# Optimization experiments

Measured on AMD Instinct MI355X. Metric: run time of the kernel, lower is better.

The kernel has to match this reference:

```python
import jax, jax.numpy as jnp
import numpy as np
from jax import lax

B, S, H = 2, 2048, 768
FF = 1536
E = 8
TOP_K = 2


def setup_inputs() -> dict:
    key = jax.random.key(0)
    k1, k2, k3, k4 = jax.random.split(key, 4)
    hidden_states = jax.random.normal(k1, (B, S, H), dtype=jnp.float32)
    # torch init: weight.normal_() for experts; nn.Linear default init for gate (approx normal here is fine for a numerics baseline)
    gate_w = jax.random.normal(k2, (E, H), dtype=jnp.float32) * 0.02
    w_fc = jax.random.normal(k3, (E, FF, H), dtype=jnp.float32) * 0.02
    w_proj = jax.random.normal(k4, (E, H, FF), dtype=jnp.float32) * 0.02
    return {"hidden_states": hidden_states, "gate_w": gate_w, "w_fc": w_fc, "w_proj": w_proj}


def reference(hidden_states, gate_w, w_fc, w_proj):
    b, s, h = hidden_states.shape
    x = hidden_states.reshape(-1, h)                      # [T, H]
    # --- top-k gating (logits in float32, as in the torch code) ---
    logits = (x @ gate_w.T).astype(jnp.float32)           # [T, E]
    top_logits, top_idx = lax.top_k(logits, TOP_K)        # [T, K]
    gates = jax.nn.softmax(top_logits, axis=1).astype(x.dtype)  # [T, K]
    # combined per-token/per-expert gate: g[t,e] = sum_k gates[t,k]*[idx[t,k]==e]
    onehot = jax.nn.one_hot(top_idx, E, dtype=x.dtype)    # [T, K, E]
    g = jnp.einsum('tk,tke->te', gates, onehot)           # [T, E]
    # --- experts: gather + per-expert GEMM + gated scatter-add combine ---
    # Equivalent math: tokens with zero gate for expert e contribute nothing,
    # so compute each expert on all tokens and weight by g[:, e].
    out = jnp.zeros_like(x)
    for e in range(E):  # fixed small loop over experts (structurally distinct weights)
        hmid = jax.nn.gelu(x @ w_fc[e].T, approximate=False)   # [T, FF] (torch gelu = erf form)
        out = out + g[:, e:e + 1] * (hmid @ w_proj[e].T)       # [T, H]
    out = out.reshape(b, s, h)
    return out, logits
```

## Files before the change

### kernel.cpp

```cpp
#include <hip/hip_runtime.h>
#include <hip/hip_bf16.h>
#include <math.h>
#include <stdint.h>

#define TOKENS 4096
#define HDIM   768
#define FFDIM  1536
#define NEXP   8
#define NCT    12
#define WMAX   768
#define GEMM_GRID 768

typedef __attribute__((ext_vector_type(8))) short bf16x8;
typedef __attribute__((ext_vector_type(4))) float f32x4;

__device__ __forceinline__ unsigned short f2bf(float f) {
    union { float f; uint32_t u; } c; c.f = f;
    uint32_t u = c.u;
    uint32_t r = (u + 0x7FFFu + ((u >> 16) & 1u)) >> 16;
    return (unsigned short)r;
}

__device__ __forceinline__ void gload_lds16(const void* g, void* l) {
    __builtin_amdgcn_global_load_lds(
        (const __attribute__((address_space(1))) void*)g,
        (__attribute__((address_space(3))) void*)l, 16, 0, 0);
}

__global__ void cast_bf16_2(const float* __restrict__ s1, unsigned short* __restrict__ d1,
                            const float* __restrict__ s2, unsigned short* __restrict__ d2,
                            int n4) {
    int stride = gridDim.x * blockDim.x;
    for (int i = blockIdx.x * blockDim.x + threadIdx.x; i < 2 * n4; i += stride) {
        const float4* s = (i < n4) ? (const float4*)s1 : (const float4*)s2;
        ushort4* d = (i < n4) ? (ushort4*)d1 : (ushort4*)d2;
        int j = (i < n4) ? i : i - n4;
        float4 v = s[j];
        ushort4 o;
        o.x = f2bf(v.x); o.y = f2bf(v.y); o.z = f2bf(v.z); o.w = f2bf(v.w);
        d[j] = o;
    }
}

__global__ __launch_bounds__(256) void gating(
    const float* __restrict__ x, const float* __restrict__ gw,
    float* __restrict__ logits,
    int* __restrict__ tok_e, float* __restrict__ tok_g,
    unsigned short* __restrict__ x_bf, float* __restrict__ outp)
{
    float4 zz = make_float4(0.f, 0.f, 0.f, 0.f);
#pragma unroll
    for (int j = 0; j < 3; j++)
        ((float4*)outp)[blockIdx.x * 768 + j * 256 + threadIdx.x] = zz;

    int t = blockIdx.x * 4 + (threadIdx.x >> 6);
    int lane = threadIdx.x & 63;
    const float4* xt = (const float4*)(x + (size_t)t * HDIM);
    const float4* gw4 = (const float4*)gw;
    ushort4* xbt = (ushort4*)(x_bf + (size_t)t * HDIM);
    float acc[NEXP];
#pragma unroll
    for (int e = 0; e < NEXP; e++) acc[e] = 0.f;
#pragma unroll
    for (int it = 0; it < 3; it++) {
        int i = lane + it * 64;
        float4 xv = xt[i];
        ushort4 o;
        o.x = f2bf(xv.x); o.y = f2bf(xv.y); o.z = f2bf(xv.z); o.w = f2bf(xv.w);
        xbt[i] = o;
#pragma unroll
        for (int e = 0; e < NEXP; e++) {
            float4 wv = gw4[e * 192 + i];
            acc[e] += xv.x * wv.x + xv.y * wv.y + xv.z * wv.z + xv.w * wv.w;
        }
    }
#pragma unroll
    for (int e = 0; e < NEXP; e++) {
#pragma unroll
        for (int off = 32; off > 0; off >>= 1)
            acc[e] += __shfl_xor(acc[e], off);
    }
    if (lane == 0) {
        float4 l0 = make_float4(acc[0], acc[1], acc[2], acc[3]);
        float4 l1 = make_float4(acc[4], acc[5], acc[6], acc[7]);
        float4* lp = (float4*)(logits + (size_t)t * NEXP);
        lp[0] = l0; lp[1] = l1;
        int i0 = 0; float v0 = acc[0];
#pragma unroll
        for (int e = 1; e < NEXP; e++) if (acc[e] > v0) { v0 = acc[e]; i0 = e; }
        int i1 = -1; float v1 = -3.4e38f;
#pragma unroll
        for (int e = 0; e < NEXP; e++) if (e != i0 && acc[e] > v1) { v1 = acc[e]; i1 = e; }
        float g0 = 1.f / (1.f + expf(v1 - v0));
        tok_e[t * 2] = i0; tok_e[t * 2 + 1] = i1;
        tok_g[t * 2] = g0; tok_g[t * 2 + 1] = 1.f - g0;
    }
}

__global__ __launch_bounds__(1024) void build_lists(
    const int* __restrict__ tok_e, const float* __restrict__ tok_g,
    int* __restrict__ counts, int* __restrict__ bases, int* __restrict__ fill,
    int* __restrict__ work,
    int* __restrict__ entries, float* __restrict__ gates)
{
    __shared__ unsigned long long wlo[16], whi[16];
    __shared__ int scnt[8];
    int tid = threadIdx.x;
    int lane = tid & 63, wid = tid >> 6;

    int eL[8]; float gL[8];
    int4 ea = ((const int4*)tok_e)[tid * 2];
    int4 eb = ((const int4*)tok_e)[tid * 2 + 1];
    float4 ga = ((const float4*)tok_g)[tid * 2];
    float4 gb = ((const float4*)tok_g)[tid * 2 + 1];
    eL[0] = ea.x; eL[1] = ea.y; eL[2] = ea.z; eL[3] = ea.w;
    eL[4] = eb.x; eL[5] = eb.y; eL[6] = eb.z; eL[7] = eb.w;
    gL[0] = ga.x; gL[1] = ga.y; gL[2] = ga.z; gL[3] = ga.w;
    gL[4] = gb.x; gL[5] = gb.y; gL[6] = gb.z; gL[7] = gb.w;

    unsigned long long clo = 0, chi = 0;
#pragma unroll
    for (int j = 0; j < 8; j++) {
        int e = eL[j];
        unsigned long long one = 1ull << ((e & 3) * 16);
        if (e < 4) clo += one; else chi += one;
    }
    unsigned long long ilo = clo, ihi = chi;
#pragma unroll
    for (int s = 1; s < 64; s <<= 1) {
        unsigned long long t1 = __shfl_up(ilo, s);
        unsigned long long t2 = __shfl_up(ihi, s);
        if (lane >= s) { ilo += t1; ihi += t2; }
    }
    if (lane == 63) { wlo[wid] = ilo; whi[wid] = ihi; }
    __syncthreads();
    if (tid == 0) {
        unsigned long long rl = 0, rh = 0;
#pragma unroll
        for (int i = 0; i < 16; i++) {
            unsigned long long a = wlo[i], b = whi[i];
            wlo[i] = rl; whi[i] = rh;
            rl += a; rh += b;
        }
        int c[8];
#pragma unroll
        for (int e = 0; e < 4; e++) {
            c[e]     = (int)((rl >> (e * 16)) & 0xFFFF);
            c[e + 4] = (int)((rh >> (e * 16)) & 0xFFFF);
        }
        int b = 0;
#pragma unroll
        for (int e = 0; e < NEXP; e++) {
            scnt[e] = c[e]; counts[e] = c[e]; bases[e] = b; b += c[e];
            fill[e] = ((c[e] + 127) >> 7) * NCT;
        }
    }
    __syncthreads();
    if (tid < NEXP * NCT) {
        int e = tid / NCT, ct = tid % NCT;
        int rts = (scnt[e] + 127) >> 7;
        for (int r = 0; r < rts; r++)
            work[(ct * rts + r) * 8 + e] = (ct << 20) | (e << 16) | (r << 7);
    }
    unsigned long long rlo = wlo[wid] + (ilo - clo);
    unsigned long long rhi = whi[wid] + (ihi - chi);
#pragma unroll
    for (int j = 0; j < 8; j++) {
        int e = eL[j];
        int sh = (e & 3) * 16;
        unsigned long long one = 1ull << sh;
        int slot;
        if (e < 4) { slot = (int)((rlo >> sh) & 0xFFFF); rlo += one; }
        else       { slot = (int)((rhi >> sh) & 0xFFFF); rhi += one; }
        entries[e * TOKENS + slot] = tid * 8 + j;
        gates[e * TOKENS + slot]   = gL[j];
    }
}

template<int KD, int ND, int TN, bool IS_FC>
__global__ __launch_bounds__(256) void moe_gemm(
    const unsigned short* __restrict__ Asrc,
    const unsigned short* __restrict__ Bsrc,
    const int* __restrict__ counts,
    const int* __restrict__ bases,
    const int* __restrict__ fill,
    const int* __restrict__ work,
    const int* __restrict__ entries,
    const float* __restrict__ gates,
    unsigned short* __restrict__ hmid,
    float* __restrict__ outp)
{
    constexpr int AJ = TN / 32;
    constexpr int CB = TN / 32;
    int bkt = blockIdx.x & 7;
    int nfill = fill[bkt];

    int tid = threadIdx.x;
    int w = tid >> 6;
    int l = tid & 63;
    int sg = l & 7;
    int lr8 = l >> 3;
    int lo = l & 15;
    int q  = l >> 4;
    int wr = w >> 1, wc = w & 1;

    __shared__ __align__(16) unsigned short sA[128 * 64];
    __shared__ __align__(16) unsigned short sB[TN * 64];

    int aOff[4][2], bOff[AJ][2];
#pragma unroll
    for (int i = 0; i < 4; i++) {
        int m = wr * 64 + i * 16 + lo;
#pragma unroll
        for (int s = 0; s < 2; s++)
            aOff[i][s] = m * 64 + ((s * 4 + q) ^ (m & 7)) * 8;
    }
#pragma unroll
    for (int j = 0; j < AJ; j++) {
        int n = wc * (TN / 2) + j * 16 + lo;
#pragma unroll
        for (int s = 0; s < 2; s++)
            bOff[j][s] = n * 64 + ((s * 4 + q) ^ (n & 7)) * 8;
    }

    for (int p = blockIdx.x >> 3; p < nfill; p += GEMM_GRID / 8) {
        int pk   = work[p * 8 + bkt];
        int ct   = pk >> 20;
        int e    = (pk >> 16) & 0xF;
        int row0 = pk & 0xFFFF;
        int n_e  = counts[e];
        int ebase = bases[e];
        int n0 = ct * TN;
        const int* lst = entries + e * TOKENS;

        const unsigned short* Ag[4];
        int aLds[4];
#pragma unroll
        for (int c = 0; c < 4; c++) {
            int rr = w * 32 + c * 8 + lr8;
            int gr = row0 + rr;
            int id = gr < n_e ? gr : n_e - 1;
            size_t arow = IS_FC ? (size_t)(lst[id] >> 1) : (size_t)(ebase + id);
            Ag[c] = Asrc + arow * KD + (size_t)((sg ^ (rr & 7)) * 8);
            aLds[c] = (w * 32 + c * 8) * 64;
        }
        const unsigned short* Bg[CB];
        int bLds[CB];
#pragma unroll
        for (int c = 0; c < CB; c++) {
            int rr = w * (TN / 4) + c * 8 + lr8;
            Bg[c] = Bsrc + ((size_t)e * ND + n0 + rr) * KD + (size_t)((sg ^ (rr & 7)) * 8);
            bLds[c] = (w * (TN / 4) + c * 8) * 64;
        }

        f32x4 acc[4][AJ];
#pragma unroll
        for (int i = 0; i < 4; i++)
#pragma unroll
            for (int j = 0; j < AJ; j++) acc[i][j] = (f32x4){0.f, 0.f, 0.f, 0.f};

        for (int k0 = 0; k0 < KD; k0 += 64) {
#pragma unroll
            for (int c = 0; c < 4; c++) gload_lds16(Ag[c] + k0, sA + aLds[c]);
#pragma unroll
            for (int c = 0; c < CB; c++) gload_lds16(Bg[c] + k0, sB + bLds[c]);
            __syncthreads();
#pragma unroll
            for (int s = 0; s < 2; s++) {
                bf16x8 a[4], b[AJ];
#pragma unroll
                for (int i = 0; i < 4; i++) a[i] = *(const bf16x8*)(sA + aOff[i][s]);
#pragma unroll
                for (int j = 0; j < AJ; j++) b[j] = *(const bf16x8*)(sB + bOff[j][s]);
#pragma unroll
                for (int i = 0; i < 4; i++)
#pragma unroll
                    for (int j = 0; j < AJ; j++)
                        acc[i][j] = __builtin_amdgcn_mfma_f32_16x16x32_bf16(a[i], b[j], acc[i][j], 0, 0, 0);
            }
            __syncthreads();
        }

#pragma unroll
        for (int i = 0; i < 4; i++) {
            int rowB = row0 + wr * 64 + i * 16 + q * 4;
#pragma unroll
            for (int rr = 0; rr < 4; rr++) {
                int orow = rowB + rr;
                if (orow < n_e) {
                    if (IS_FC) {
                        size_t hrow = (size_t)(ebase + orow);
#pragma unroll
                        for (int j = 0; j < AJ; j++) {
                            float v = acc[i][j][rr];
                            v = 0.5f * v * (1.f + erff(v * 0.70710678118654752f));
                            hmid[hrow * ND + n0 + wc * (TN / 2) + j * 16 + lo] = f2bf(v);
                        }
                    } else {
                        int token = lst[orow] >> 1;
                        float g = gates[e * TOKENS + orow];
#pragma unroll
                        for (int j = 0; j < AJ; j++) {
                            atomicAdd(&outp[(size_t)token * ND + n0 + wc * (TN / 2) + j * 16 + lo],
                                      acc[i][j][rr] * g);
                        }
                    }
                }
            }
        }
    }
}

extern "C" void kernel_launch(void* const* d_in, const int* in_sizes, int n_in,
                              void* d_out, int out_size, void* d_ws, size_t ws_size,
                              hipStream_t stream) {
    const float* x     = (const float*)d_in[0];
    const float* gw    = (const float*)d_in[1];
    const float* wfc   = (const float*)d_in[2];
    const float* wproj = (const float*)d_in[3];
    float* outp   = (float*)d_out;
    float* logits = outp + (size_t)TOKENS * HDIM;

    char* ws = (char*)d_ws;
    int*   counts  = (int*)ws;
    int*   bases   = (int*)(ws + 64);
    int*   fill    = (int*)(ws + 128);
    int*   work    = (int*)(ws + 256);
    size_t off = 256 + (size_t)WMAX * 8 * 4;
    int*   entries = (int*)(ws + off);
    float* gates   = (float*)(ws + off + NEXP * TOKENS * 4);
    off += 2ull * NEXP * TOKENS * 4;
    int*   tok_e   = (int*)(ws + off);   off += (size_t)TOKENS * 2 * 4;
    float* tok_g   = (float*)(ws + off); off += (size_t)TOKENS * 2 * 4;
    unsigned short* x_bf   = (unsigned short*)(ws + off); off += (size_t)TOKENS * HDIM * 2;
    unsigned short* wfc_bf = (unsigned short*)(ws + off); off += (size_t)NEXP * FFDIM * HDIM * 2;
    unsigned short* wpj_bf = (unsigned short*)(ws + off); off += (size_t)NEXP * HDIM * FFDIM * 2;
    unsigned short* hmid   = (unsigned short*)(ws + off);

    cast_bf16_2<<<2048, 256, 0, stream>>>(wfc, wfc_bf, wproj, wpj_bf,
                                          NEXP * FFDIM * HDIM / 4);
    gating<<<TOKENS / 4, 256, 0, stream>>>(x, gw, logits, tok_e, tok_g, x_bf, outp);
    build_lists<<<1, 1024, 0, stream>>>(tok_e, tok_g, counts, bases, fill, work,
                                        entries, gates);
    moe_gemm<HDIM, FFDIM, 128, true ><<<GEMM_GRID, 256, 0, stream>>>(
        x_bf, wfc_bf, counts, bases, fill, work, entries, gates, hmid, outp);
    moe_gemm<FFDIM, HDIM, 64, false><<<GEMM_GRID, 256, 0, stream>>>(
        hmid, wpj_bf, counts, bases, fill, work, entries, gates, hmid, outp);
}
```

Before: 235.0 us.

## Replace list-building kernel with atomic slot assignment in gating and derived schedule

Drops the single-block build_lists kernel. Gating now appends each token to per-expert lists with global atomics, and the counters are zeroed inside the cast kernel. The GEMM blocks derive their work tiles, expert base offsets and row ranges straight from the counts, which removes one launch and the precomputed work table. The grid grows to 1024 blocks with a launch_bounds occupancy hint. The token order inside each expert list becomes nondeterministic, so the atomicAdd accumulation order changes, and the many contended atomics on eight counters may add some serialization.

```diff
diff --git a/kernel.cpp b/kernel.cpp
--- a/kernel.cpp
+++ b/kernel.cpp
@@ -7,9 +7,8 @@
 #define HDIM   768
 #define FFDIM  1536
 #define NEXP   8
-#define NCT    12
-#define WMAX   768
-#define GEMM_GRID 768
+#define GEMM_GRID 1024
+#define SLOTS (GEMM_GRID / 8)
 
 typedef __attribute__((ext_vector_type(8))) short bf16x8;
 typedef __attribute__((ext_vector_type(4))) float f32x4;
@@ -29,7 +28,8 @@
 
 __global__ void cast_bf16_2(const float* __restrict__ s1, unsigned short* __restrict__ d1,
                             const float* __restrict__ s2, unsigned short* __restrict__ d2,
-                            int n4) {
+                            int n4, int* __restrict__ counts) {
+    if (blockIdx.x == 0 && threadIdx.x < NEXP) counts[threadIdx.x] = 0;
     int stride = gridDim.x * blockDim.x;
     for (int i = blockIdx.x * blockDim.x + threadIdx.x; i < 2 * n4; i += stride) {
         const float4* s = (i < n4) ? (const float4*)s1 : (const float4*)s2;
@@ -45,7 +45,7 @@
 __global__ __launch_bounds__(256) void gating(
     const float* __restrict__ x, const float* __restrict__ gw,
     float* __restrict__ logits,
-    int* __restrict__ tok_e, float* __restrict__ tok_g,
+    int* __restrict__ counts, int* __restrict__ entries, float* __restrict__ gates,
     unsigned short* __restrict__ x_bf, float* __restrict__ outp)
 {
     float4 zz = make_float4(0.f, 0.f, 0.f, 0.f);
@@ -92,99 +92,20 @@
 #pragma unroll
         for (int e = 0; e < NEXP; e++) if (e != i0 && acc[e] > v1) { v1 = acc[e]; i1 = e; }
         float g0 = 1.f / (1.f + expf(v1 - v0));
-        tok_e[t * 2] = i0; tok_e[t * 2 + 1] = i1;
-        tok_g[t * 2] = g0; tok_g[t * 2 + 1] = 1.f - g0;
-    }
-}
-
-__global__ __launch_bounds__(1024) void build_lists(
-    const int* __restrict__ tok_e, const float* __restrict__ tok_g,
-    int* __restrict__ counts, int* __restrict__ bases, int* __restrict__ fill,
-    int* __restrict__ work,
-    int* __restrict__ entries, float* __restrict__ gates)
-{
-    __shared__ unsigned long long wlo[16], whi[16];
-    __shared__ int scnt[8];
-    int tid = threadIdx.x;
-    int lane = tid & 63, wid = tid >> 6;
-
-    int eL[8]; float gL[8];
-    int4 ea = ((const int4*)tok_e)[tid * 2];
-    int4 eb = ((const int4*)tok_e)[tid * 2 + 1];
-    float4 ga = ((const float4*)tok_g)[tid * 2];
-    float4 gb = ((const float4*)tok_g)[tid * 2 + 1];
-    eL[0] = ea.x; eL[1] = ea.y; eL[2] = ea.z; eL[3] = ea.w;
-    eL[4] = eb.x; eL[5] = eb.y; eL[6] = eb.z; eL[7] = eb.w;
-    gL[0] = ga.x; gL[1] = ga.y; gL[2] = ga.z; gL[3] = ga.w;
-    gL[4] = gb.x; gL[5] = gb.y; gL[6] = gb.z; gL[7] = gb.w;
-
-    unsigned long long clo = 0, chi = 0;
-#pragma unroll
-    for (int j = 0; j < 8; j++) {
-        int e = eL[j];
-        unsigned long long one = 1ull << ((e & 3) * 16);
-        if (e < 4) clo += one; else chi += one;
-    }
-    unsigned long long ilo = clo, ihi = chi;
-#pragma unroll
-    for (int s = 1; s < 64; s <<= 1) {
-        unsigned long long t1 = __shfl_up(ilo, s);
-        unsigned long long t2 = __shfl_up(ihi, s);
-        if (lane >= s) { ilo += t1; ihi += t2; }
-    }
-    if (lane == 63) { wlo[wid] = ilo; whi[wid] = ihi; }
-    __syncthreads();
-    if (tid == 0) {
-        unsigned long long rl = 0, rh = 0;
-#pragma unroll
-        for (int i = 0; i < 16; i++) {
-            unsigned long long a = wlo[i], b = whi[i];
-            wlo[i] = rl; whi[i] = rh;
-            rl += a; rh += b;
-        }
-        int c[8];
-#pragma unroll
-        for (int e = 0; e < 4; e++) {
-            c[e]     = (int)((rl >> (e * 16)) & 0xFFFF);
-            c[e + 4] = (int)((rh >> (e * 16)) & 0xFFFF);
-        }
-        int b = 0;
-#pragma unroll
-        for (int e = 0; e < NEXP; e++) {
-            scnt[e] = c[e]; counts[e] = c[e]; bases[e] = b; b += c[e];
-            fill[e] = ((c[e] + 127) >> 7) * NCT;
-        }
-    }
-    __syncthreads();
-    if (tid < NEXP * NCT) {
-        int e = tid / NCT, ct = tid % NCT;
-        int rts = (scnt[e] + 127) >> 7;
-        for (int r = 0; r < rts; r++)
-            work[(ct * rts + r) * 8 + e] = (ct << 20) | (e << 16) | (r << 7);
-    }
-    unsigned long long rlo = wlo[wid] + (ilo - clo);
-    unsigned long long rhi = whi[wid] + (ihi - chi);
-#pragma unroll
-    for (int j = 0; j < 8; j++) {
-        int e = eL[j];
-        int sh = (e & 3) * 16;
-        unsigned long long one = 1ull << sh;
-        int slot;
-        if (e < 4) { slot = (int)((rlo >> sh) & 0xFFFF); rlo += one; }
-        else       { slot = (int)((rhi >> sh) & 0xFFFF); rhi += one; }
-        entries[e * TOKENS + slot] = tid * 8 + j;
-        gates[e * TOKENS + slot]   = gL[j];
-    }
-}
-
-template<int KD, int ND, int TN, bool IS_FC>
-__global__ __launch_bounds__(256) void moe_gemm(
+        int s0 = atomicAdd(&counts[i0], 1);
+        int s1 = atomicAdd(&counts[i1], 1);
+        entries[i0 * TOKENS + s0] = t * 2;
+        gates  [i0 * TOKENS + s0] = g0;
+        entries[i1 * TOKENS + s1] = t * 2 + 1;
+        gates  [i1 * TOKENS + s1] = 1.f - g0;
+    }
+}
+
+template<int KD, int ND, int TN, int NCTP, bool IS_FC>
+__global__ __launch_bounds__(256, 4) void moe_gemm(
     const unsigned short* __restrict__ Asrc,
     const unsigned short* __restrict__ Bsrc,
     const int* __restrict__ counts,
-    const int* __restrict__ bases,
-    const int* __restrict__ fill,
-    const int* __restrict__ work,
     const int* __restrict__ entries,
     const float* __restrict__ gates,
     unsigned short* __restrict__ hmid,
@@ -192,8 +113,20 @@
 {
     constexpr int AJ = TN / 32;
     constexpr int CB = TN / 32;
-    int bkt = blockIdx.x & 7;
-    int nfill = fill[bkt];
+    int bkt  = blockIdx.x & 7;
+    int slot = blockIdx.x >> 3;
+
+    int cs[NEXP];
+#pragma unroll
+    for (int e = 0; e < NEXP; e++) cs[e] = counts[e];
+    int n_e = cs[bkt];
+    int rts = (n_e + 127) >> 7;
+    int nfill = rts * NCTP;
+    if (slot >= nfill) return;
+    int ebase = 0;
+#pragma unroll
+    for (int e = 0; e < NEXP; e++) if (e < bkt) ebase += cs[e];
+    const int* lst = entries + bkt * TOKENS;
 
     int tid = threadIdx.x;
     int w = tid >> 6;
@@ -223,15 +156,11 @@
             bOff[j][s] = n * 64 + ((s * 4 + q) ^ (n & 7)) * 8;
     }
 
-    for (int p = blockIdx.x >> 3; p < nfill; p += GEMM_GRID / 8) {
-        int pk   = work[p * 8 + bkt];
-        int ct   = pk >> 20;
-        int e    = (pk >> 16) & 0xF;
-        int row0 = pk & 0xFFFF;
-        int n_e  = counts[e];
-        int ebase = bases[e];
+    for (int p = slot; p < nfill; p += SLOTS) {
+        int ct   = p / rts;
+        int r    = p - ct * rts;
+        int row0 = r << 7;
         int n0 = ct * TN;
-        const int* lst = entries + e * TOKENS;
 
         const unsigned short* Ag[4];
         int aLds[4];
@@ -249,7 +178,7 @@
 #pragma unroll
         for (int c = 0; c < CB; c++) {
             int rr = w * (TN / 4) + c * 8 + lr8;
-            Bg[c] = Bsrc + ((size_t)e * ND + n0 + rr) * KD + (size_t)((sg ^ (rr & 7)) * 8);
+            Bg[c] = Bsrc + ((size_t)bkt * ND + n0 + rr) * KD + (size_t)((sg ^ (rr & 7)) * 8);
             bLds[c] = (w * (TN / 4) + c * 8) * 64;
         }
 
@@ -298,7 +227,7 @@
                         }
                     } else {
                         int token = lst[orow] >> 1;
-                        float g = gates[e * TOKENS + orow];
+                        float g = gates[bkt * TOKENS + orow];
 #pragma unroll
                         for (int j = 0; j < AJ; j++) {
                             atomicAdd(&outp[(size_t)token * ND + n0 + wc * (TN / 2) + j * 16 + lo],
@@ -323,27 +252,21 @@
 
     char* ws = (char*)d_ws;
     int*   counts  = (int*)ws;
-    int*   bases   = (int*)(ws + 64);
-    int*   fill    = (int*)(ws + 128);
-    int*   work    = (int*)(ws + 256);
-    size_t off = 256 + (size_t)WMAX * 8 * 4;
+    size_t off = 256;
     int*   entries = (int*)(ws + off);
     float* gates   = (float*)(ws + off + NEXP * TOKENS * 4);
     off += 2ull * NEXP * TOKENS * 4;
-    int*   tok_e   = (int*)(ws + off);   off += (size_t)TOKENS * 2 * 4;
-    float* tok_g   = (float*)(ws + off); off += (size_t)TOKENS * 2 * 4;
     unsigned short* x_bf   = (unsigned short*)(ws + off); off += (size_t)TOKENS * HDIM * 2;
     unsigned short* wfc_bf = (unsigned short*)(ws + off); off += (size_t)NEXP * FFDIM * HDIM * 2;
     unsigned short* wpj_bf = (unsigned short*)(ws + off); off += (size_t)NEXP * HDIM * FFDIM * 2;
     unsigned short* hmid   = (unsigned short*)(ws + off);
 
     cast_bf16_2<<<2048, 256, 0, stream>>>(wfc, wfc_bf, wproj, wpj_bf,
-                                          NEXP * FFDIM * HDIM / 4);
-    gating<<<TOKENS / 4, 256, 0, stream>>>(x, gw, logits, tok_e, tok_g, x_bf, outp);
-    build_lists<<<1, 1024, 0, stream>>>(tok_e, tok_g, counts, bases, fill, work,
-                                        entries, gates);
-    moe_gemm<HDIM, FFDIM, 128, true ><<<GEMM_GRID, 256, 0, stream>>>(
-        x_bf, wfc_bf, counts, bases, fill, work, entries, gates, hmid, outp);
-    moe_gemm<FFDIM, HDIM, 64, false><<<GEMM_GRID, 256, 0, stream>>>(
-        hmid, wpj_bf, counts, bases, fill, work, entries, gates, hmid, outp);
-}
+                                          NEXP * FFDIM * HDIM / 4, counts);
+    gating<<<TOKENS / 4, 256, 0, stream>>>(x, gw, logits, counts, entries, gates,
+                                           x_bf, outp);
+    moe_gemm<HDIM, FFDIM, 128, FFDIM / 128, true ><<<GEMM_GRID, 256, 0, stream>>>(
+        x_bf, wfc_bf, counts, entries, gates, hmid, outp);
+    moe_gemm<FFDIM, HDIM, 64, HDIM / 64, false><<<GEMM_GRID, 256, 0, stream>>>(
+        hmid, wpj_bf, counts, entries, gates, hmid, outp);
+}
```

Result: slower. 324.8 us (+38.2%).

## Derive MoE GEMM tile schedule in-kernel from counts and enlarge grid

Applied to the files above, without the earlier changes.

Removes the precomputed work list, bases and fill arrays from build_lists. Each GEMM block now reads the expert counts, computes its expert base offset and tile index arithmetically, and exits early when it has no tiles. The grid grows from 768 to 1024 blocks with launch_bounds(256,4), so each expert gets more parallel slots and occupancy is hinted. This trades some redundant per-block scalar work for less build_lists work and fewer dependent global loads per tile, at the risk of register pressure from the occupancy hint.

```diff
diff --git a/kernel.cpp b/kernel.cpp
--- a/kernel.cpp
+++ b/kernel.cpp
@@ -7,9 +7,8 @@
 #define HDIM   768
 #define FFDIM  1536
 #define NEXP   8
-#define NCT    12
-#define WMAX   768
-#define GEMM_GRID 768
+#define GEMM_GRID 1024
+#define SLOTS (GEMM_GRID / 8)
 
 typedef __attribute__((ext_vector_type(8))) short bf16x8;
 typedef __attribute__((ext_vector_type(4))) float f32x4;
@@ -99,12 +98,10 @@
 
 __global__ __launch_bounds__(1024) void build_lists(
     const int* __restrict__ tok_e, const float* __restrict__ tok_g,
-    int* __restrict__ counts, int* __restrict__ bases, int* __restrict__ fill,
-    int* __restrict__ work,
+    int* __restrict__ counts,
     int* __restrict__ entries, float* __restrict__ gates)
 {
     __shared__ unsigned long long wlo[16], whi[16];
-    __shared__ int scnt[8];
     int tid = threadIdx.x;
     int lane = tid & 63, wid = tid >> 6;
 
@@ -142,26 +139,13 @@
             wlo[i] = rl; whi[i] = rh;
             rl += a; rh += b;
         }
-        int c[8];
 #pragma unroll
         for (int e = 0; e < 4; e++) {
-            c[e]     = (int)((rl >> (e * 16)) & 0xFFFF);
-            c[e + 4] = (int)((rh >> (e * 16)) & 0xFFFF);
-        }
-        int b = 0;
-#pragma unroll
-        for (int e = 0; e < NEXP; e++) {
-            scnt[e] = c[e]; counts[e] = c[e]; bases[e] = b; b += c[e];
-            fill[e] = ((c[e] + 127) >> 7) * NCT;
+            counts[e]     = (int)((rl >> (e * 16)) & 0xFFFF);
+            counts[e + 4] = (int)((rh >> (e * 16)) & 0xFFFF);
         }
     }
     __syncthreads();
-    if (tid < NEXP * NCT) {
-        int e = tid / NCT, ct = tid % NCT;
-        int rts = (scnt[e] + 127) >> 7;
-        for (int r = 0; r < rts; r++)
-            work[(ct * rts + r) * 8 + e] = (ct << 20) | (e << 16) | (r << 7);
-    }
     unsigned long long rlo = wlo[wid] + (ilo - clo);
     unsigned long long rhi = whi[wid] + (ihi - chi);
 #pragma unroll
@@ -177,14 +161,11 @@
     }
 }
 
-template<int KD, int ND, int TN, bool IS_FC>
-__global__ __launch_bounds__(256) void moe_gemm(
+template<int KD, int ND, int TN, int NCTP, bool IS_FC>
+__global__ __launch_bounds__(256, 4) void moe_gemm(
     const unsigned short* __restrict__ Asrc,
     const unsigned short* __restrict__ Bsrc,
     const int* __restrict__ counts,
-    const int* __restrict__ bases,
-    const int* __restrict__ fill,
-    const int* __restrict__ work,
     const int* __restrict__ entries,
     const float* __restrict__ gates,
     unsigned short* __restrict__ hmid,
@@ -192,8 +173,20 @@
 {
     constexpr int AJ = TN / 32;
     constexpr int CB = TN / 32;
-    int bkt = blockIdx.x & 7;
-    int nfill = fill[bkt];
+    int bkt  = blockIdx.x & 7;
+    int slot = blockIdx.x >> 3;
+
+    int cs[NEXP];
+#pragma unroll
+    for (int e = 0; e < NEXP; e++) cs[e] = counts[e];
+    int n_e = cs[bkt];
+    int rts = (n_e + 127) >> 7;
+    int nfill = rts * NCTP;
+    if (slot >= nfill) return;
+    int ebase = 0;
+#pragma unroll
+    for (int e = 0; e < NEXP; e++) if (e < bkt) ebase += cs[e];
+    const int* lst = entries + bkt * TOKENS;
 
     int tid = threadIdx.x;
     int w = tid >> 6;
@@ -223,15 +216,11 @@
             bOff[j][s] = n * 64 + ((s * 4 + q) ^ (n & 7)) * 8;
     }
 
-    for (int p = blockIdx.x >> 3; p < nfill; p += GEMM_GRID / 8) {
-        int pk   = work[p * 8 + bkt];
-        int ct   = pk >> 20;
-        int e    = (pk >> 16) & 0xF;
-        int row0 = pk & 0xFFFF;
-        int n_e  = counts[e];
-        int ebase = bases[e];
+    for (int p = slot; p < nfill; p += SLOTS) {
+        int ct   = p / rts;
+        int r    = p - ct * rts;
+        int row0 = r << 7;
         int n0 = ct * TN;
-        const int* lst = entries + e * TOKENS;
 
         const unsigned short* Ag[4];
         int aLds[4];
@@ -249,7 +238,7 @@
 #pragma unroll
         for (int c = 0; c < CB; c++) {
             int rr = w * (TN / 4) + c * 8 + lr8;
-            Bg[c] = Bsrc + ((size_t)e * ND + n0 + rr) * KD + (size_t)((sg ^ (rr & 7)) * 8);
+            Bg[c] = Bsrc + ((size_t)bkt * ND + n0 + rr) * KD + (size_t)((sg ^ (rr & 7)) * 8);
             bLds[c] = (w * (TN / 4) + c * 8) * 64;
         }
 
@@ -298,7 +287,7 @@
                         }
                     } else {
                         int token = lst[orow] >> 1;
-                        float g = gates[e * TOKENS + orow];
+                        float g = gates[bkt * TOKENS + orow];
 #pragma unroll
                         for (int j = 0; j < AJ; j++) {
                             atomicAdd(&outp[(size_t)token * ND + n0 + wc * (TN / 2) + j * 16 + lo],
@@ -323,10 +312,7 @@
 
     char* ws = (char*)d_ws;
     int*   counts  = (int*)ws;
-    int*   bases   = (int*)(ws + 64);
-    int*   fill    = (int*)(ws + 128);
-    int*   work    = (int*)(ws + 256);
-    size_t off = 256 + (size_t)WMAX * 8 * 4;
+    size_t off = 256;
     int*   entries = (int*)(ws + off);
     float* gates   = (float*)(ws + off + NEXP * TOKENS * 4);
     off += 2ull * NEXP * TOKENS * 4;
@@ -340,10 +326,9 @@
     cast_bf16_2<<<2048, 256, 0, stream>>>(wfc, wfc_bf, wproj, wpj_bf,
                                           NEXP * FFDIM * HDIM / 4);
     gating<<<TOKENS / 4, 256, 0, stream>>>(x, gw, logits, tok_e, tok_g, x_bf, outp);
-    build_lists<<<1, 1024, 0, stream>>>(tok_e, tok_g, counts, bases, fill, work,
-                                        entries, gates);
-    moe_gemm<HDIM, FFDIM, 128, true ><<<GEMM_GRID, 256, 0, stream>>>(
-        x_bf, wfc_bf, counts, bases, fill, work, entries, gates, hmid, outp);
-    moe_gemm<FFDIM, HDIM, 64, false><<<GEMM_GRID, 256, 0, stream>>>(
-        hmid, wpj_bf, counts, bases, fill, work, entries, gates, hmid, outp);
-}
+    build_lists<<<1, 1024, 0, stream>>>(tok_e, tok_g, counts, entries, gates);
+    moe_gemm<HDIM, FFDIM, 128, FFDIM / 128, true ><<<GEMM_GRID, 256, 0, stream>>>(
+        x_bf, wfc_bf, counts, entries, gates, hmid, outp);
+    moe_gemm<FFDIM, HDIM, 64, HDIM / 64, false><<<GEMM_GRID, 256, 0, stream>>>(
+        hmid, wpj_bf, counts, entries, gates, hmid, outp);
+}
```

Result: slower. 242.6 us (+3.2%).
